# Optimization experiments

Hardware: AMD Instinct MI355X
Metric: run time of the kernel (lower is better)

The kernel has to match this reference:

```python
import jax, jax.numpy as jnp
import numpy as np

D_MODEL = 1024
NUM_HEADS = 16
D_K = D_MODEL // NUM_HEADS
LOCAL_WINDOW = 16
LOCALITY_STRENGTH = 2.0


def _xavier(key, shape):
    fan_in, fan_out = shape[1], shape[0]
    a = jnp.sqrt(6.0 / (fan_in + fan_out))
    return jax.random.uniform(key, shape, jnp.float32, -a, a)


def setup_inputs() -> dict:
    key = jax.random.key(0)
    ks = jax.random.split(key, 9)
    B, S = 4, 2048
    query = jax.random.normal(ks[0], (B, S, D_MODEL), jnp.float32)
    key_t = jax.random.normal(ks[1], (B, S, D_MODEL), jnp.float32)
    value = jax.random.normal(ks[2], (B, S, D_MODEL), jnp.float32)
    wq = _xavier(ks[3], (D_MODEL, D_MODEL))
    wk = _xavier(ks[4], (D_MODEL, D_MODEL))
    wv = _xavier(ks[5], (D_MODEL, D_MODEL))
    wo = _xavier(ks[6], (D_MODEL, D_MODEL))
    bq = jnp.zeros((D_MODEL,), jnp.float32)
    bk = jnp.zeros((D_MODEL,), jnp.float32)
    bv = jnp.zeros((D_MODEL,), jnp.float32)
    bo = jnp.zeros((D_MODEL,), jnp.float32)
    # learned local relative-position bias, length 2*W+1; randomize so grads/math are nontrivial
    local_bias = 0.02 * jax.random.normal(ks[7], (2 * LOCAL_WINDOW + 1,), jnp.float32)
    return {"query": query, "key": key_t, "value": value,
            "wq": wq, "bq": bq, "wk": wk, "bk": bk, "wv": wv, "bv": bv,
            "wo": wo, "bo": bo, "local_bias": local_bias}


def _local_bias_matrix(local_bias, seq_len):
    # bias[i, j] = local_bias[j - i + W] if |j - i| <= W else 0  (banded)
    i = jnp.arange(seq_len)
    rel = i[None, :] - i[:, None]                 # [S, S]
    valid = jnp.abs(rel) <= LOCAL_WINDOW
    idx = jnp.clip(rel + LOCAL_WINDOW, 0, 2 * LOCAL_WINDOW)
    return jnp.where(valid, local_bias[idx], 0.0)  # [S, S]


def reference(query, key, value, wq, bq, wk, bk, wv, bv, wo, bo, local_bias):
    B, S, _ = query.shape
    H, Dk = NUM_HEADS, D_K
    q = (query @ wq.T + bq).reshape(B, S, H, Dk).transpose(0, 2, 1, 3)  # [B,H,S,Dk]
    k = (key @ wk.T + bk).reshape(B, S, H, Dk).transpose(0, 2, 1, 3)
    v = (value @ wv.T + bv).reshape(B, S, H, Dk).transpose(0, 2, 1, 3)
    scores = jnp.einsum('bhqd,bhkd->bhqk', q, k) / jnp.sqrt(jnp.float32(Dk))
    bias = _local_bias_matrix(local_bias, S)       # [S,S], broadcasts over [B,H]
    scores = scores + LOCALITY_STRENGTH * bias
    attn = jax.nn.softmax(scores, axis=-1)
    out = jnp.einsum('bhqk,bhkd->bhqd', attn, v)   # [B,H,S,Dk]
    out = out.transpose(0, 2, 1, 3).reshape(B, S, H * Dk)
    return out @ wo.T + bo
```

## Files before the change

### kernel.cpp

```cpp
#include <hip/hip_runtime.h>
#include <hip/hip_bf16.h>
#include <stdint.h>

typedef __bf16 bf16_t;
typedef bf16_t bf16x8 __attribute__((ext_vector_type(8)));
typedef bf16_t bf16x4 __attribute__((ext_vector_type(4)));
typedef float f32x4 __attribute__((ext_vector_type(4)));

#define LOG2E 1.44269504088896340736f

__device__ __forceinline__ void gld16(const void* g, void* l) {
  __builtin_amdgcn_global_load_lds(
      (__attribute__((address_space(1))) void*)(void*)(g),
      (__attribute__((address_space(3))) void*)(l), 16, 0, 0);
}

__device__ __forceinline__ int swz(int byteoff) {
  return byteoff ^ (((byteoff >> 7) & 7) << 4);
}

__global__ __launch_bounds__(256) void cvt7_kernel(
    const float* __restrict__ a0, const float* __restrict__ a1, const float* __restrict__ a2,
    const float* __restrict__ w0, const float* __restrict__ w1,
    const float* __restrict__ w2, const float* __restrict__ w3,
    bf16_t* __restrict__ e0, bf16_t* __restrict__ e1, bf16_t* __restrict__ e2,
    bf16_t* __restrict__ f0, bf16_t* __restrict__ f1,
    bf16_t* __restrict__ f2, bf16_t* __restrict__ f3) {
  const float* s;
  bf16_t* d;
  int i, stride;
  if (blockIdx.x < 3072) {
    const int t = blockIdx.x >> 10;
    s = (t == 0) ? a0 : ((t == 1) ? a1 : a2);
    d = (t == 0) ? e0 : ((t == 1) ? e1 : e2);
    i = (blockIdx.x & 1023) * 256 + threadIdx.x;
    stride = 1024 * 256;
  } else {
    const int b = blockIdx.x - 3072;
    const int t = b >> 7;
    s = (t == 0) ? w0 : ((t == 1) ? w1 : ((t == 2) ? w2 : w3));
    d = (t == 0) ? f0 : ((t == 1) ? f1 : ((t == 2) ? f2 : f3));
    i = (b & 127) * 256 + threadIdx.x;
    stride = 128 * 256;
  }
#pragma unroll
  for (int u = 0; u < 8; ++u, i += stride) {
    const float4 v = reinterpret_cast<const float4*>(s)[i];
    bf16x4 o;
    o[0] = (bf16_t)v.x; o[1] = (bf16_t)v.y; o[2] = (bf16_t)v.z; o[3] = (bf16_t)v.w;
    reinterpret_cast<bf16x4*>(d)[i] = o;
  }
}

#define GBM 128
#define GBN 128
#define GBK 64

__device__ __forceinline__ void gemm_core(
    const bf16_t* __restrict__ A, const bf16_t* __restrict__ W,
    bf16_t* As, bf16_t* Bs, int m0, int n0, int K,
    int wm, int wn, int rr, int kk8, f32x4 acc[4][4]) {
  const int tid = threadIdx.x;
  const int t16 = tid * 16;
  int srow[4], scb[4];
#pragma unroll
  for (int i = 0; i < 4; ++i) {
    const int so = swz(i * 4096 + t16);
    srow[i] = so >> 7;
    scb[i] = so & 127;
  }
  const char* Ab = (const char*)A;
  const char* Wb = (const char*)W;
  const int nk = K / GBK;

#define GSTAGE(bufsel, kk0)                                                    \
  {                                                                            \
    char* Al = (char*)As + (bufsel) * 16384 + t16;                             \
    char* Bl = (char*)Bs + (bufsel) * 16384 + t16;                             \
    _Pragma("unroll")                                                          \
    for (int i = 0; i < 4; ++i) {                                              \
      gld16(Ab + ((size_t)(m0 + srow[i]) * K + (kk0)) * 2 + scb[i], Al + i * 4096); \
      gld16(Wb + ((size_t)(n0 + srow[i]) * K + (kk0)) * 2 + scb[i], Bl + i * 4096); \
    }                                                                          \
  }

  GSTAGE(0, 0)
  for (int t = 0; t < nk; ++t) {
    const int b = t & 1;
    asm volatile("s_waitcnt vmcnt(0)" ::: "memory");
    __builtin_amdgcn_s_barrier();
    __builtin_amdgcn_sched_barrier(0);
    GSTAGE(b ^ 1, ((t + 1) & (nk - 1)) * GBK)
    const char* Abl = (const char*)As + b * 16384;
    const char* Bbl = (const char*)Bs + b * 16384;
#pragma unroll
    for (int kk = 0; kk < 2; ++kk) {
      bf16x8 a[4], bb[4];
#pragma unroll
      for (int i = 0; i < 4; ++i)
        a[i] = *reinterpret_cast<const bf16x8*>(
            Abl + swz((wm + i * 16 + rr) * 128 + (kk * 32 + kk8) * 2));
#pragma unroll
      for (int i = 0; i < 4; ++i)
        bb[i] = *reinterpret_cast<const bf16x8*>(
            Bbl + swz((wn + i * 16 + rr) * 128 + (kk * 32 + kk8) * 2));
      __builtin_amdgcn_s_setprio(1);
#pragma unroll
      for (int i = 0; i < 4; ++i)
#pragma unroll
        for (int j = 0; j < 4; ++j)
          acc[i][j] = __builtin_amdgcn_mfma_f32_16x16x32_bf16(a[i], bb[j], acc[i][j], 0, 0, 0);
      __builtin_amdgcn_s_setprio(0);
    }
  }
#undef GSTAGE
}

__global__ __launch_bounds__(256) void gemm_qkv(
    const bf16_t* __restrict__ Xq, const bf16_t* __restrict__ Xk, const bf16_t* __restrict__ Xv,
    const bf16_t* __restrict__ Wq, const bf16_t* __restrict__ Wk, const bf16_t* __restrict__ Wv,
    const float* __restrict__ bq, const float* __restrict__ bk, const float* __restrict__ bv,
    bf16_t* __restrict__ Qo, bf16_t* __restrict__ Ko, bf16_t* __restrict__ Vo,
    int M, int N, int K) {
  const int z = blockIdx.z;
  const bf16_t* A = (z == 0) ? Xq : ((z == 1) ? Xk : Xv);
  const bf16_t* W = (z == 0) ? Wq : ((z == 1) ? Wk : Wv);
  const float* bias = (z == 0) ? bq : ((z == 1) ? bk : bv);
  bf16_t* Out = (z == 0) ? Qo : ((z == 1) ? Ko : Vo);

  __shared__ bf16_t As[2 * GBM * GBK];
  __shared__ bf16_t Bs[2 * GBN * GBK];
  const int tid = threadIdx.x;
  const int lane = tid & 63;
  const int w = tid >> 6;
  const int m0 = blockIdx.x * GBM;
  const int n0 = blockIdx.y * GBN;
  const int wm = (w >> 1) * 64;
  const int wn = (w & 1) * 64;
  const int rr = lane & 15;
  const int kk8 = (lane >> 4) * 8;

  f32x4 acc[4][4] = {};
  gemm_core(A, W, As, Bs, m0, n0, K, wm, wn, rr, kk8, acc);

  const int rg = (lane >> 4) * 4;
#pragma unroll
  for (int i = 0; i < 4; ++i) {
#pragma unroll
    for (int j = 0; j < 4; ++j) {
      const int col = n0 + wn + j * 16 + rr;
      const float bi = bias[col];
      if (z == 2) {
        const int row0 = m0 + wm + i * 16 + rg;
        const int b_ = row0 >> 11, s_ = row0 & 2047;
        const int h_ = col >> 6, d_ = col & 63;
        const int k64 = s_ & 63;
        const int sl = (k64 & 32) | ((k64 & 12) << 1) | ((k64 & 16) >> 2);
        const int scol = (s_ & ~63) | sl;
        bf16x4 pack;
#pragma unroll
        for (int r = 0; r < 4; ++r) pack[r] = (bf16_t)(acc[i][j][r] + bi);
        *reinterpret_cast<bf16x4*>(&Out[((size_t)((b_ * 16 + h_) * 64 + d_)) * 2048 + scol]) = pack;
      } else {
        const float scale = (z == 0) ? (0.125f * LOG2E) : 1.0f;
#pragma unroll
        for (int r = 0; r < 4; ++r) {
          const int row = m0 + wm + i * 16 + rg + r;
          const int b_ = row >> 11, s_ = row & 2047;
          const int h_ = col >> 6, d_ = col & 63;
          Out[((size_t)((b_ * 16 + h_) * 2048 + s_)) * 64 + d_] = (bf16_t)((acc[i][j][r] + bi) * scale);
        }
      }
    }
  }
}

__global__ __launch_bounds__(256) void gemm_o(
    const bf16_t* __restrict__ A, const bf16_t* __restrict__ W,
    const float* __restrict__ bias, float* __restrict__ Out,
    int M, int N, int K) {
  __shared__ bf16_t As[2 * GBM * GBK];
  __shared__ bf16_t Bs[2 * GBN * GBK];
  const int tid = threadIdx.x;
  const int lane = tid & 63;
  const int w = tid >> 6;
  const int m0 = blockIdx.x * GBM;
  const int n0 = blockIdx.y * GBN;
  const int wm = (w >> 1) * 64;
  const int wn = (w & 1) * 64;
  const int rr = lane & 15;
  const int kk8 = (lane >> 4) * 8;

  f32x4 acc[4][4] = {};
  gemm_core(A, W, As, Bs, m0, n0, K, wm, wn, rr, kk8, acc);

  const int rg = (lane >> 4) * 4;
#pragma unroll
  for (int i = 0; i < 4; ++i)
#pragma unroll
    for (int j = 0; j < 4; ++j) {
      const int col = n0 + wn + j * 16 + rr;
      const float bi = bias[col];
#pragma unroll
      for (int r = 0; r < 4; ++r) {
        const int row = m0 + wm + i * 16 + rg + r;
        Out[(size_t)row * N + col] = acc[i][j][r] + bi;
      }
    }
}

#define QT 256
#define KT 64

__global__ __launch_bounds__(256, 2) void attn_kernel(
    const bf16_t* __restrict__ Qg, const bf16_t* __restrict__ Kg,
    const bf16_t* __restrict__ Vtg, const float* __restrict__ lb,
    bf16_t* __restrict__ Og) {
  const int S = 2048;
  __shared__ bf16_t Qs[QT * 64];
  __shared__ bf16_t Ks[KT * 64];
  __shared__ bf16_t Vts[64 * KT];
  __shared__ float lbs[33];

  const int tid = threadIdx.x, lane = tid & 63, w = tid >> 6;
  const int bh = blockIdx.x;
  const int qt0 = blockIdx.y * QT;
  const int b_ = bh >> 4, h_ = bh & 15;

  const char* Qb = (const char*)(Qg + (size_t)bh * S * 64);
  const char* Kb = (const char*)(Kg + (size_t)bh * S * 64);
  const char* Vtb = (const char*)(Vtg + (size_t)bh * 64 * S);

#pragma unroll
  for (int i = 0; i < 8; ++i) {
    const int off = i * 4096 + tid * 16;
    gld16(Qb + (size_t)qt0 * 128 + swz(off), (char*)Qs + off);
  }
  if (tid < 33) lbs[tid] = lb[tid];

  const int L0 = tid * 16;
  const int W0 = swz(L0), W1 = swz(L0 + 4096);
  const int vd0 = L0 >> 7, vcb = L0 & 127;
  int4 kr0, kr1, vr0, vr1;

#define LOADKV(t)                                                              \
  {                                                                            \
    const char* kp = Kb + (size_t)(t) * 8192;                                  \
    kr0 = *reinterpret_cast<const int4*>(kp + L0);                             \
    kr1 = *reinterpret_cast<const int4*>(kp + L0 + 4096);                      \
    const char* vp = Vtb + (size_t)(t) * 128;                                  \
    vr0 = *reinterpret_cast<const int4*>(vp + (size_t)vd0 * 4096 + vcb);       \
    vr1 = *reinterpret_cast<const int4*>(vp + (size_t)(vd0 + 32) * 4096 + vcb);\
  }
#define WRITEKV()                                                              \
  {                                                                            \
    *reinterpret_cast<int4*>((char*)Ks + W0) = kr0;                            \
    *reinterpret_cast<int4*>((char*)Ks + W1) = kr1;                            \
    *reinterpret_cast<int4*>((char*)Vts + W0) = vr0;                           \
    *reinterpret_cast<int4*>((char*)Vts + W1) = vr1;                           \
  }

  LOADKV(0)
  __syncthreads();

  const int rr = lane & 15;
  const int kk8 = (lane >> 4) * 8;
  const int rg = (lane >> 4) * 4;

  bf16x8 qf[4][2];
#pragma unroll
  for (int qg = 0; qg < 4; ++qg)
#pragma unroll
    for (int kk = 0; kk < 2; ++kk) {
      const int off = (w * 64 + qg * 16 + rr) * 128 + (kk * 32 + kk8) * 2;
      qf[qg][kk] = *reinterpret_cast<const bf16x8*>((const char*)Qs + swz(off));
    }

  f32x4 oacc[4][4] = {};
  float lrowp[4] = {0.f, 0.f, 0.f, 0.f};

  for (int kt = 0; kt < S / KT; ++kt) {
    WRITEKV()
    __syncthreads();
    LOADKV((kt + 1) & 31)

    bf16x8 kf[4][2];
#pragma unroll
    for (int ni = 0; ni < 4; ++ni)
#pragma unroll
      for (int kk = 0; kk < 2; ++kk) {
        const int off = (ni * 16 + rr) * 128 + (kk * 32 + kk8) * 2;
        kf[ni][kk] = *reinterpret_cast<const bf16x8*>((const char*)Ks + swz(off));
      }
    bf16x8 vf[2][4];
#pragma unroll
    for (int kk = 0; kk < 2; ++kk)
#pragma unroll
      for (int nd = 0; nd < 4; ++nd) {
        const int off = (nd * 16 + rr) * 128 + (kk * 32 + kk8) * 2;
        vf[kk][nd] = *reinterpret_cast<const bf16x8*>((const char*)Vts + swz(off));
      }

    const int kbase = kt * KT;
#pragma unroll
    for (int qg = 0; qg < 4; ++qg) {
      f32x4 sc[4];
      __builtin_amdgcn_s_setprio(1);
#pragma unroll
      for (int ni = 0; ni < 4; ++ni) {
        f32x4 z = {0.f, 0.f, 0.f, 0.f};
#pragma unroll
        for (int kk = 0; kk < 2; ++kk)
          z = __builtin_amdgcn_mfma_f32_16x16x32_bf16(kf[ni][kk], qf[qg][kk], z, 0, 0, 0);
        sc[ni] = z;
      }
      __builtin_amdgcn_s_setprio(0);

      const int qlo = qt0 + w * 64 + qg * 16;
      if (kbase + KT + 16 > qlo && kbase < qlo + 16 + 16) {
        const int q = qlo + rr;
#pragma unroll
        for (int ni = 0; ni < 4; ++ni)
#pragma unroll
          for (int r = 0; r < 4; ++r) {
            const int rel = (kbase + ni * 16 + rg + r) - q;
            if (rel >= -16 && rel <= 16)
              sc[ni][r] += (2.0f * LOG2E) * lbs[rel + 16];
          }
      }

      bf16x8 paf[2];
      float ps0 = 0.f, ps1 = 0.f;
#pragma unroll
      for (int ni = 0; ni < 4; ++ni) {
        const float p0 = exp2f(sc[ni][0]);
        const float p1 = exp2f(sc[ni][1]);
        const float p2 = exp2f(sc[ni][2]);
        const float p3 = exp2f(sc[ni][3]);
        ps0 += p0 + p2;
        ps1 += p1 + p3;
        paf[ni >> 1][(ni & 1) * 4 + 0] = (bf16_t)p0;
        paf[ni >> 1][(ni & 1) * 4 + 1] = (bf16_t)p1;
        paf[ni >> 1][(ni & 1) * 4 + 2] = (bf16_t)p2;
        paf[ni >> 1][(ni & 1) * 4 + 3] = (bf16_t)p3;
      }
      lrowp[qg] += ps0 + ps1;

      __builtin_amdgcn_s_setprio(1);
#pragma unroll
      for (int kk = 0; kk < 2; ++kk)
#pragma unroll
        for (int nd = 0; nd < 4; ++nd)
          oacc[qg][nd] = __builtin_amdgcn_mfma_f32_16x16x32_bf16(paf[kk], vf[kk][nd], oacc[qg][nd], 0, 0, 0);
      __builtin_amdgcn_s_setprio(0);
    }
    __syncthreads();
  }

#pragma unroll
  for (int qg = 0; qg < 4; ++qg) {
    float t = lrowp[qg];
    t += __shfl_xor(t, 16, 64);
    t += __shfl_xor(t, 32, 64);
    float lf[4];
#pragma unroll
    for (int r = 0; r < 4; ++r)
      lf[r] = __shfl(t, (lane & 48) | (rg + r), 64);
#pragma unroll
    for (int nd = 0; nd < 4; ++nd)
#pragma unroll
      for (int r = 0; r < 4; ++r) {
        const int srow = qt0 + w * 64 + qg * 16 + rg + r;
        const int d = nd * 16 + rr;
        const float v = oacc[qg][nd][r] / lf[r];
        Og[((size_t)(b_ * 2048 + srow)) * 1024 + h_ * 64 + d] = (bf16_t)v;
      }
  }
}

extern "C" void kernel_launch(void* const* d_in, const int* in_sizes, int n_in,
                              void* d_out, int out_size, void* d_ws, size_t ws_size,
                              hipStream_t stream) {
  const float* q32 = (const float*)d_in[0];
  const float* k32 = (const float*)d_in[1];
  const float* v32 = (const float*)d_in[2];
  const float* wq = (const float*)d_in[3];
  const float* bq = (const float*)d_in[4];
  const float* wk = (const float*)d_in[5];
  const float* bk = (const float*)d_in[6];
  const float* wv = (const float*)d_in[7];
  const float* bv = (const float*)d_in[8];
  const float* wo = (const float*)d_in[9];
  const float* bo = (const float*)d_in[10];
  const float* lb = (const float*)d_in[11];

  const int M = 8192, N = 1024, K = 1024;
  const size_t REG = (size_t)M * N * 2;

  char* ws = (char*)d_ws;
  bf16_t* Xq = (bf16_t*)(ws + 0 * REG);
  bf16_t* Xk = (bf16_t*)(ws + 1 * REG);
  bf16_t* Xv = (bf16_t*)(ws + 2 * REG);
  bf16_t* Qb = (bf16_t*)(ws + 3 * REG);
  bf16_t* Wqb = (bf16_t*)(ws + 4 * REG);
  bf16_t* Wkb = Wqb + (size_t)N * K;
  bf16_t* Wvb = Wkb + (size_t)N * K;
  bf16_t* Wob = Wvb + (size_t)N * K;
  bf16_t* Kb = Xq;
  bf16_t* Vt = Xk;
  bf16_t* attn = Xv;

  cvt7_kernel<<<dim3(3584), dim3(256), 0, stream>>>(
      q32, k32, v32, wq, wk, wv, wo, Xq, Xk, Xv, Wqb, Wkb, Wvb, Wob);

  gemm_qkv<<<dim3(M / GBM, N / GBN, 3), 256, 0, stream>>>(
      Xq, Xk, Xv, Wqb, Wkb, Wvb, bq, bk, bv, Qb, Kb, Vt, M, N, K);

  attn_kernel<<<dim3(64, 2048 / QT), 256, 0, stream>>>(Qb, Kb, Vt, lb, attn);

  gemm_o<<<dim3(M / GBM, N / GBN), 256, 0, stream>>>(attn, Wob, bo, (float*)d_out, M, N, K);
}
```

Before: 229.8 us.

## Batch QK MFMAs across all query groups before softmax and PV

Restructures the attention inner loop so all 4 query groups' QK^T MFMAs are issued together, then bias, exp2 and P conversion for all groups, then all PV MFMAs, instead of interleaving per group. This gives longer MFMA bursts and moves the V fragment loads later, aiming to overlap them with the exp work. It holds all scores and P fragments live at once, which raises register pressure, so the min-blocks-per-CU hint of 2 in launch_bounds is dropped, risking lower occupancy or spills.

```diff
diff --git a/kernel.cpp b/kernel.cpp
--- a/kernel.cpp
+++ b/kernel.cpp
@@ -212,7 +212,7 @@
 #define QT 256
 #define KT 64
 
-__global__ __launch_bounds__(256, 2) void attn_kernel(
+__global__ __launch_bounds__(256) void attn_kernel(
     const bf16_t* __restrict__ Qg, const bf16_t* __restrict__ Kg,
     const bf16_t* __restrict__ Vtg, const float* __restrict__ lb,
     bf16_t* __restrict__ Og) {
@@ -292,6 +292,59 @@
         const int off = (ni * 16 + rr) * 128 + (kk * 32 + kk8) * 2;
         kf[ni][kk] = *reinterpret_cast<const bf16x8*>((const char*)Ks + swz(off));
       }
+
+    const int kbase = kt * KT;
+
+    f32x4 sc[4][4];
+    __builtin_amdgcn_s_setprio(1);
+#pragma unroll
+    for (int qg = 0; qg < 4; ++qg)
+#pragma unroll
+      for (int ni = 0; ni < 4; ++ni) {
+        f32x4 z = {0.f, 0.f, 0.f, 0.f};
+#pragma unroll
+        for (int kk = 0; kk < 2; ++kk)
+          z = __builtin_amdgcn_mfma_f32_16x16x32_bf16(kf[ni][kk], qf[qg][kk], z, 0, 0, 0);
+        sc[qg][ni] = z;
+      }
+    __builtin_amdgcn_s_setprio(0);
+
+#pragma unroll
+    for (int qg = 0; qg < 4; ++qg) {
+      const int qlo = qt0 + w * 64 + qg * 16;
+      if (kbase + KT + 16 > qlo && kbase < qlo + 16 + 16) {
+        const int q = qlo + rr;
+#pragma unroll
+        for (int ni = 0; ni < 4; ++ni)
+#pragma unroll
+          for (int r = 0; r < 4; ++r) {
+            const int rel = (kbase + ni * 16 + rg + r) - q;
+            if (rel >= -16 && rel <= 16)
+              sc[qg][ni][r] += (2.0f * LOG2E) * lbs[rel + 16];
+          }
+      }
+    }
+
+    bf16x8 paf[4][2];
+#pragma unroll
+    for (int qg = 0; qg < 4; ++qg) {
+      float ps0 = 0.f, ps1 = 0.f;
+#pragma unroll
+      for (int ni = 0; ni < 4; ++ni) {
+        const float p0 = exp2f(sc[qg][ni][0]);
+        const float p1 = exp2f(sc[qg][ni][1]);
+        const float p2 = exp2f(sc[qg][ni][2]);
+        const float p3 = exp2f(sc[qg][ni][3]);
+        ps0 += p0 + p2;
+        ps1 += p1 + p3;
+        paf[qg][ni >> 1][(ni & 1) * 4 + 0] = (bf16_t)p0;
+        paf[qg][ni >> 1][(ni & 1) * 4 + 1] = (bf16_t)p1;
+        paf[qg][ni >> 1][(ni & 1) * 4 + 2] = (bf16_t)p2;
+        paf[qg][ni >> 1][(ni & 1) * 4 + 3] = (bf16_t)p3;
+      }
+      lrowp[qg] += ps0 + ps1;
+    }
+
     bf16x8 vf[2][4];
 #pragma unroll
     for (int kk = 0; kk < 2; ++kk)
@@ -301,59 +354,16 @@
         vf[kk][nd] = *reinterpret_cast<const bf16x8*>((const char*)Vts + swz(off));
       }
 
-    const int kbase = kt * KT;
-#pragma unroll
-    for (int qg = 0; qg < 4; ++qg) {
-      f32x4 sc[4];
-      __builtin_amdgcn_s_setprio(1);
-#pragma unroll
-      for (int ni = 0; ni < 4; ++ni) {
-        f32x4 z = {0.f, 0.f, 0.f, 0.f};
-#pragma unroll
-        for (int kk = 0; kk < 2; ++kk)
-          z = __builtin_amdgcn_mfma_f32_16x16x32_bf16(kf[ni][kk], qf[qg][kk], z, 0, 0, 0);
-        sc[ni] = z;
-      }
-      __builtin_amdgcn_s_setprio(0);
-
-      const int qlo = qt0 + w * 64 + qg * 16;
-      if (kbase + KT + 16 > qlo && kbase < qlo + 16 + 16) {
-        const int q = qlo + rr;
-#pragma unroll
-        for (int ni = 0; ni < 4; ++ni)
-#pragma unroll
-          for (int r = 0; r < 4; ++r) {
-            const int rel = (kbase + ni * 16 + rg + r) - q;
-            if (rel >= -16 && rel <= 16)
-              sc[ni][r] += (2.0f * LOG2E) * lbs[rel + 16];
-          }
-      }
-
-      bf16x8 paf[2];
-      float ps0 = 0.f, ps1 = 0.f;
-#pragma unroll
-      for (int ni = 0; ni < 4; ++ni) {
-        const float p0 = exp2f(sc[ni][0]);
-        const float p1 = exp2f(sc[ni][1]);
-        const float p2 = exp2f(sc[ni][2]);
-        const float p3 = exp2f(sc[ni][3]);
-        ps0 += p0 + p2;
-        ps1 += p1 + p3;
-        paf[ni >> 1][(ni & 1) * 4 + 0] = (bf16_t)p0;
-        paf[ni >> 1][(ni & 1) * 4 + 1] = (bf16_t)p1;
-        paf[ni >> 1][(ni & 1) * 4 + 2] = (bf16_t)p2;
-        paf[ni >> 1][(ni & 1) * 4 + 3] = (bf16_t)p3;
-      }
-      lrowp[qg] += ps0 + ps1;
-
-      __builtin_amdgcn_s_setprio(1);
-#pragma unroll
-      for (int kk = 0; kk < 2; ++kk)
+    __builtin_amdgcn_s_setprio(1);
+#pragma unroll
+    for (int kk = 0; kk < 2; ++kk)
+#pragma unroll
+      for (int qg = 0; qg < 4; ++qg)
 #pragma unroll
         for (int nd = 0; nd < 4; ++nd)
-          oacc[qg][nd] = __builtin_amdgcn_mfma_f32_16x16x32_bf16(paf[kk], vf[kk][nd], oacc[qg][nd], 0, 0, 0);
-      __builtin_amdgcn_s_setprio(0);
-    }
+          oacc[qg][nd] = __builtin_amdgcn_mfma_f32_16x16x32_bf16(paf[qg][kk], vf[kk][nd], oacc[qg][nd], 0, 0, 0);
+    __builtin_amdgcn_s_setprio(0);
+
     __syncthreads();
   }
 
```

After: 287.7 us. 25.2% more time.
